# Optimization experiments

Measured on AMD Instinct MI355X. Metric: run time of the kernel, lower is better.

The kernel has to match this reference:

```python
import jax, jax.numpy as jnp
import numpy as np

# Architecture constants (from init_kwargs)
A, L, NCF = 200, 10, 9            # num_agent, in_len, num_control_features
D_MODEL, N_HEADS = 1024, 4
HEAD_DIM = D_MODEL // N_HEADS      # 256 (the module's 'head_dim')
PER_HEAD = HEAD_DIM // N_HEADS     # 64 (effective per-head dim after rearrange)
SCALE = HEAD_DIM ** -0.5           # module scales by head_dim**-0.5
N = A * L + NCF                    # 2009 tokens


def _build_mask():
    # block-diagonal agent mask: eye(A) repeat_interleaved L on both axes,
    # then zero-padded by NCF rows/cols for control features
    m = np.kron(np.eye(A, dtype=np.float32), np.ones((L, L), dtype=np.float32))
    m = np.pad(m, ((0, NCF), (0, NCF)))
    return jnp.asarray(m)  # [N, N]

_MASK = _build_mask()


def setup_inputs() -> dict:
    key = jax.random.key(0)
    k0, k1, k2, k3 = jax.random.split(key, 4)
    x = jax.random.normal(k0, (4, N, D_MODEL), jnp.float32)
    W_qkv = jax.random.normal(k1, (D_MODEL, HEAD_DIM * 3), jnp.float32) * 0.02
    W_qk_self = jax.random.normal(k2, (D_MODEL, HEAD_DIM * 2), jnp.float32) * 0.02
    W_out = jax.random.normal(k3, (HEAD_DIM, D_MODEL), jnp.float32) * 0.02
    b_out = jnp.zeros((D_MODEL,), jnp.float32)
    return {"x": x, "W_qkv": W_qkv, "W_qk_self": W_qk_self,
            "W_out": W_out, "b_out": b_out}


def _heads(t, b, n):
    # 'b n (h d) -> b h n d' with h = N_HEADS
    return t.reshape(b, n, N_HEADS, PER_HEAD).transpose(0, 2, 1, 3)


def reference(x, W_qkv, W_qk_self, W_out, b_out):
    b, n, _ = x.shape
    q, k, v = jnp.split(x @ W_qkv, 3, axis=-1)          # each [b, n, HEAD_DIM]
    q, k, v = _heads(q, b, n), _heads(k, b, n), _heads(v, b, n)  # [b,h,n,d]
    q_self, k_self = jnp.split(x @ W_qk_self, 2, axis=-1)
    q_self, k_self = _heads(q_self, b, n), _heads(k_self, b, n)

    dots = jnp.einsum('bhnd,bhmd->bhnm', q, k) * SCALE
    dots_self = jnp.einsum('bhnd,bhmd->bhnm', q_self, k_self) * SCALE
    dots_all = _MASK * dots_self + (1.0 - _MASK) * dots  # blend via block mask
    attn = jax.nn.softmax(dots_all, axis=-1)             # [b,h,n,n]

    out = jnp.einsum('bhnm,bhmd->bhnd', attn, v)
    out = out.transpose(0, 2, 1, 3).reshape(b, n, HEAD_DIM)  # 'b h n d -> b n (h d)'
    out = out @ W_out + b_out                            # to_out (dropout=0)
    return out, attn
```

## Files before the change

kernel.cpp:

```cpp
#include <hip/hip_runtime.h>

typedef unsigned short u16;
typedef unsigned int u32;
typedef short short8 __attribute__((ext_vector_type(8)));
typedef float f32x4 __attribute__((ext_vector_type(4)));
typedef float f32x16 __attribute__((ext_vector_type(16)));
typedef float float4a __attribute__((ext_vector_type(4), aligned(4)));

#define NTOK 2009
#define M8   8036
#define DMOD 1024
#define PKBH 129024

static __device__ __forceinline__ u16 f2bf(float f) {
  unsigned int x = __float_as_uint(f);
  x += 0x7fffu + ((x >> 16) & 1u);
  return (u16)(x >> 16);
}
static __device__ __forceinline__ float bf2f(u16 u) {
  return __uint_as_float((unsigned int)u << 16);
}
static __device__ __forceinline__ u32 pk2(float a, float b) {
  return (u32)f2bf(a) | ((u32)f2bf(b) << 16);
}
static __device__ __forceinline__ u32 cvtpk(float a, float b) {
  u32 d;
  asm("v_cvt_pk_bf16_f32 %0, %1, %2" : "=v"(d) : "v"(a), "v"(b));
  return d;
}

__global__ void k_conv_x(const float* __restrict__ x, u16* __restrict__ xb) {
  int i = blockIdx.x * 256 + threadIdx.x;
  float4 v = ((const float4*)x)[i];
  unsigned int a = (unsigned int)f2bf(v.x) | ((unsigned int)f2bf(v.y) << 16);
  unsigned int b = (unsigned int)f2bf(v.z) | ((unsigned int)f2bf(v.w) << 16);
  ((uint2*)xb)[i] = make_uint2(a, b);
}

__global__ void k_conv_wcat(const float* __restrict__ Wqkv, const float* __restrict__ Wqs,
                            u16* __restrict__ WtCat) {
  int i = blockIdx.x * 256 + threadIdx.x;
  int n = i >> 10, k = i & 1023;
  float v = (n < 768) ? Wqkv[k * 768 + n] : Wqs[k * 512 + (n - 768)];
  WtCat[i] = f2bf(v);
}

__global__ void k_conv_wout(const float* __restrict__ Wout, u16* __restrict__ WtOut) {
  int i = blockIdx.x * 256 + threadIdx.x;
  int n = i >> 8, k = i & 255;
  WtOut[i] = f2bf(Wout[k * 1024 + n]);
}

__global__ __launch_bounds__(256) void k_gemm_proj(
    const u16* __restrict__ A, const u16* __restrict__ Bt,
    u16* __restrict__ Qp, u16* __restrict__ Kp, u16* __restrict__ Vp,
    u16* __restrict__ Qsb, u16* __restrict__ Ksb)
{
  const int K = 1024;
  __shared__ u16 Al[64][72];
  __shared__ u16 Bl[64][72];
  int mt = blockIdx.x * 64, nt = blockIdx.y * 64;
  int tid = threadIdx.x; int lane = tid & 63, wave = tid >> 6;
  int fr = lane & 15, fk = (lane >> 4) * 8;
  f32x4 acc[4];
#pragma unroll
  for (int i = 0; i < 4; ++i) acc[i] = (f32x4){0.f, 0.f, 0.f, 0.f};
  for (int kt = 0; kt < K; kt += 64) {
#pragma unroll
    for (int r = 0; r < 2; ++r) {
      int c = tid + r * 256;
      int row = c >> 3, ch = (c & 7) * 8;
      int am = mt + row; if (am >= M8) am = 0;
      *(short8*)&Al[row][ch] = *(const short8*)&A[(size_t)am * K + kt + ch];
      *(short8*)&Bl[row][ch] = *(const short8*)&Bt[(size_t)(nt + row) * K + kt + ch];
    }
    __syncthreads();
#pragma unroll
    for (int cs = 0; cs < 2; ++cs) {
      short8 bfr = *(const short8*)&Bl[wave * 16 + fr][cs * 32 + fk];
#pragma unroll
      for (int mi = 0; mi < 4; ++mi) {
        short8 afr = *(const short8*)&Al[mi * 16 + fr][cs * 32 + fk];
        acc[mi] = __builtin_amdgcn_mfma_f32_16x16x32_bf16(afr, bfr, acc[mi], 0, 0, 0);
      }
    }
    __syncthreads();
  }
  int n = nt + wave * 16 + fr;
  int g = n >> 6, d = n & 63;
  int h = g & 3, sel = g >> 2;
  float scl = (sel == 0 || sel == 3) ? 0.0625f : 1.0f;
#pragma unroll
  for (int mi = 0; mi < 4; ++mi) {
#pragma unroll
    for (int i = 0; i < 4; ++i) {
      int m = mt + mi * 16 + (lane >> 4) * 4 + i;
      if (m >= M8) continue;
      int b_ = m / NTOK, tok = m - b_ * NTOK;
      int bh = b_ * 4 + h;
      u16 val = f2bf(acc[mi][i] * scl);
      if (sel <= 1) {
        u16* dst = sel == 0 ? Qp : Kp;
        size_t idx = ((((size_t)bh * 63 + (tok >> 5)) * 4 + (d >> 4)) * 2 + ((d >> 3) & 1)) * 256
                     + (tok & 31) * 8 + (d & 7);
        dst[idx] = val;
      } else if (sel == 2) {
        size_t idx = (((((size_t)bh * 63 + (tok >> 5)) * 2 + (d >> 5)) * 2 + ((tok >> 4) & 1)) * 2
                      + ((tok >> 3) & 1)) * 256 + (d & 31) * 8 + (tok & 7);
        Vp[idx] = val;
      } else {
        u16* p = (sel == 3) ? Qsb : Ksb;
        p[((size_t)bh * NTOK + tok) * 64 + d] = val;
      }
    }
  }
}

__global__ void k_self(const u16* __restrict__ Qs, const u16* __restrict__ Ks,
                       float* __restrict__ selfS) {
  int blk = blockIdx.x;
  int bh = blk / 200, a = blk % 200;
  int t = threadIdx.x;
  if (t >= 100) return;
  int ri = t / 10, rj = t % 10;
  const u16* qp = &Qs[((size_t)bh * NTOK + a * 10 + ri) * 64];
  const u16* kp = &Ks[((size_t)bh * NTOK + a * 10 + rj) * 64];
  float s = 0.f;
#pragma unroll 8
  for (int k = 0; k < 64; ++k) s += bf2f(qp[k]) * bf2f(kp[k]);
  selfS[(size_t)blk * 100 + t] = s;
}

__global__ __launch_bounds__(256, 2) void k_attn5(
    const u16* __restrict__ Qp, const u16* __restrict__ Kp,
    const u16* __restrict__ Vp, const float* __restrict__ selfS,
    float* __restrict__ attn, u16* __restrict__ Ob)
{
  __shared__ float s_sum[4][32];
  __shared__ float s_o[4][64][32];
  __shared__ float s_p[4][1024];
  int bh = blockIdx.x;
  int qt = blockIdx.y;
  int q0 = qt * 32;
  int tid = threadIdx.x;
  int lane = tid & 63, w = tid >> 6;
  int ql = lane & 31, h = lane >> 5;
  int qg = q0 + ql;
  int lo8 = ql * 8;

  const u16* qbase = Qp + (size_t)bh * PKBH + (size_t)qt * 2048;
  const u16* kbase = Kp + (size_t)bh * PKBH;
  const u16* vbase = Vp + (size_t)bh * PKBH;

  short8 qf[4];
#pragma unroll
  for (int c = 0; c < 4; ++c)
    qf[c] = *(const short8*)&qbase[(c * 2 + h) * 256 + lo8];

  int qa = (qg < 2000) ? (qg / 10) : -1;
  int band_lo = 1 << 30, band_hi = -(1 << 30);
  if (q0 < 2000) {
    int hi_row = (q0 + 31 < 1999) ? q0 + 31 : 1999;
    band_lo = (q0 / 10) * 10;
    band_hi = (hi_row / 10) * 10 + 10;
  }
  const float* sfb = &selfS[(size_t)bh * 20000];

  int t0 = w * 16;
  int t1 = t0 + 16; if (t1 > 63) t1 = 63;

  u32 pb[16][8];
  short8 kf[4], kfn[4];

#pragma unroll
  for (int c = 0; c < 4; ++c)
    kf[c] = *(const short8*)&kbase[(size_t)t0 * 2048 + (c * 2 + h) * 256 + lo8];
  float ssum = 0.f;
#pragma unroll
  for (int i = 0; i < 16; ++i) {
    int t = t0 + i;
    if (t < t1) {
      int tn = (t + 1 < t1) ? t + 1 : t0;
#pragma unroll
      for (int c = 0; c < 4; ++c)
        kfn[c] = *(const short8*)&kbase[(size_t)tn * 2048 + (c * 2 + h) * 256 + lo8];
      f32x16 acc = {};
#pragma unroll
      for (int c = 0; c < 4; ++c)
        acc = __builtin_amdgcn_mfma_f32_32x32x16_bf16(kf[c], qf[c], acc, 0, 0, 0);
      int kt = t * 32;
      float e[16];
      if ((kt < band_hi) && (kt + 32 > band_lo)) {
#pragma unroll
        for (int r = 0; r < 16; ++r) {
          int kc = kt + (r & 3) + 8 * (r >> 2) + 4 * h;
          float sc = acc[r];
          if (qa >= 0 && kc < 2000 && (kc / 10) == qa)
            sc = sfb[qa * 100 + (qg - qa * 10) * 10 + (kc - qa * 10)];
          e[r] = __expf(sc);
        }
      } else {
#pragma unroll
        for (int r = 0; r < 16; ++r) e[r] = __expf(acc[r]);
      }
      if (t == 62) {
#pragma unroll
        for (int r = 0; r < 16; ++r) {
          int kc = kt + (r & 3) + 8 * (r >> 2) + 4 * h;
          if (kc >= NTOK) e[r] = 0.f;
        }
      }
#pragma unroll
      for (int r2 = 0; r2 < 8; ++r2) {
        pb[i][r2] = cvtpk(e[2 * r2], e[2 * r2 + 1]);
        ssum += e[2 * r2] + e[2 * r2 + 1];
      }
#pragma unroll
      for (int c = 0; c < 4; ++c) kf[c] = kfn[c];
    }
  }
  ssum += __shfl_xor(ssum, 32);
  if (lane < 32) s_sum[w][ql] = ssum;
  __syncthreads();
  float inv = 1.0f / (s_sum[0][ql] + s_sum[1][ql] + s_sum[2][ql] + s_sum[3][ql]);

  f32x16 oacc0 = {}, oacc1 = {};
  short8 vf[4], vfn[4];
#pragma unroll
  for (int idx = 0; idx < 4; ++idx)
    vf[idx] = *(const short8*)&vbase[(size_t)t0 * 2048 + (idx * 2 + h) * 256 + lo8];

  char* pl = (char*)&s_p[w][0];

#pragma unroll
  for (int i = 0; i < 16; ++i) {
    int t = t0 + i;
    if (t < t1) {
      int tn = (t + 1 < t1) ? t + 1 : t0;
#pragma unroll
      for (int idx = 0; idx < 4; ++idx)
        vfn[idx] = *(const short8*)&vbase[(size_t)tn * 2048 + (idx * 2 + h) * 256 + lo8];
      int kt = t * 32;

#pragma unroll
      for (int rq = 0; rq < 4; ++rq) {
        u32 ua = pb[i][2 * rq], ub = pb[i][2 * rq + 1];
        f32x4 v = {__uint_as_float(ua << 16) * inv,
                   __uint_as_float(ua & 0xffff0000u) * inv,
                   __uint_as_float(ub << 16) * inv,
                   __uint_as_float(ub & 0xffff0000u) * inv};
        *(f32x4*)(pl + ql * 128 + ((rq * 32 + h * 16) ^ ((ql & 7) << 4))) = v;
      }
#pragma unroll
      for (int i2 = 0; i2 < 4; ++i2) {
        int r = i2 * 8 + (lane >> 3), ch = lane & 7;
        f32x4 v = *(f32x4*)(pl + r * 128 + ((ch * 16) ^ ((r & 7) << 4)));
        int grow = q0 + r;
        int col0 = kt + ch * 4;
        if (grow < NTOK) {
          float* arow = &attn[((size_t)bh * NTOK + grow) * NTOK];
          if (col0 + 3 < NTOK) {
            *(float4a*)&arow[col0] = (float4a){v[0], v[1], v[2], v[3]};
          } else {
#pragma unroll
            for (int j = 0; j < 4; ++j)
              if (col0 + j < NTOK) arow[col0 + j] = v[j];
          }
        }
      }

      u32 p00 = __shfl_xor(pb[i][0], 32), p01 = __shfl_xor(pb[i][1], 32);
      u32 p10 = __shfl_xor(pb[i][2], 32), p11 = __shfl_xor(pb[i][3], 32);
      u32 p20 = __shfl_xor(pb[i][4], 32), p21 = __shfl_xor(pb[i][5], 32);
      u32 p30 = __shfl_xor(pb[i][6], 32), p31 = __shfl_xor(pb[i][7], 32);
      u32 b0[4], b1[4];
      b0[0] = h ? p10 : pb[i][0];  b0[1] = h ? p11 : pb[i][1];
      b0[2] = h ? pb[i][2] : p00;  b0[3] = h ? pb[i][3] : p01;
      b1[0] = h ? p30 : pb[i][4];  b1[1] = h ? p31 : pb[i][5];
      b1[2] = h ? pb[i][6] : p20;  b1[3] = h ? pb[i][7] : p21;
      short8 B0, B1;
      __builtin_memcpy(&B0, b0, 16);
      __builtin_memcpy(&B1, b1, 16);
      oacc0 = __builtin_amdgcn_mfma_f32_32x32x16_bf16(vf[0], B0, oacc0, 0, 0, 0);
      oacc1 = __builtin_amdgcn_mfma_f32_32x32x16_bf16(vf[2], B0, oacc1, 0, 0, 0);
      oacc0 = __builtin_amdgcn_mfma_f32_32x32x16_bf16(vf[1], B1, oacc0, 0, 0, 0);
      oacc1 = __builtin_amdgcn_mfma_f32_32x32x16_bf16(vf[3], B1, oacc1, 0, 0, 0);
#pragma unroll
      for (int c = 0; c < 4; ++c) vf[c] = vfn[c];
    }
  }

#pragma unroll
  for (int r = 0; r < 16; ++r) {
    int d = (r & 3) + 8 * (r >> 2) + 4 * h;
    s_o[w][d][ql] = oacc0[r];
    s_o[w][d + 32][ql] = oacc1[r];
  }
  __syncthreads();
  {
    int q = tid & 31, dg = tid >> 5;
    int qg2 = q0 + q;
    if (qg2 < NTOK) {
      float invq = 1.0f / (s_sum[0][q] + s_sum[1][q] + s_sum[2][q] + s_sum[3][q]);
      int b_ = bh >> 2, hd = bh & 3;
      u16* orow = &Ob[((size_t)(b_ * NTOK + qg2)) * 256 + hd * 64 + dg * 8];
      u32 wpk[4];
#pragma unroll
      for (int j = 0; j < 4; ++j) {
        int d = dg * 8 + 2 * j;
        float a = (s_o[0][d][q] + s_o[1][d][q] + s_o[2][d][q] + s_o[3][d][q]) * invq;
        float b = (s_o[0][d + 1][q] + s_o[1][d + 1][q] + s_o[2][d + 1][q] + s_o[3][d + 1][q]) * invq;
        wpk[j] = pk2(a, b);
      }
      *(uint4*)orow = make_uint4(wpk[0], wpk[1], wpk[2], wpk[3]);
    }
  }
}

__global__ __launch_bounds__(256) void k_gemm_out(
    const u16* __restrict__ A, const u16* __restrict__ Bt,
    const float* __restrict__ bias, float* __restrict__ C)
{
  const int K = 256;
  __shared__ u16 Al[64][72];
  __shared__ u16 Bl[64][72];
  int mt = blockIdx.x * 64, nt = blockIdx.y * 64;
  int tid = threadIdx.x; int lane = tid & 63, wave = tid >> 6;
  int fr = lane & 15, fk = (lane >> 4) * 8;
  f32x4 acc[4];
#pragma unroll
  for (int i = 0; i < 4; ++i) acc[i] = (f32x4){0.f, 0.f, 0.f, 0.f};
  for (int kt = 0; kt < K; kt += 64) {
#pragma unroll
    for (int r = 0; r < 2; ++r) {
      int c = tid + r * 256;
      int row = c >> 3, ch = (c & 7) * 8;
      int am = mt + row; if (am >= M8) am = 0;
      *(short8*)&Al[row][ch] = *(const short8*)&A[(size_t)am * K + kt + ch];
      *(short8*)&Bl[row][ch] = *(const short8*)&Bt[(size_t)(nt + row) * K + kt + ch];
    }
    __syncthreads();
#pragma unroll
    for (int cs = 0; cs < 2; ++cs) {
      short8 bfr = *(const short8*)&Bl[wave * 16 + fr][cs * 32 + fk];
#pragma unroll
      for (int mi = 0; mi < 4; ++mi) {
        short8 afr = *(const short8*)&Al[mi * 16 + fr][cs * 32 + fk];
        acc[mi] = __builtin_amdgcn_mfma_f32_16x16x32_bf16(afr, bfr, acc[mi], 0, 0, 0);
      }
    }
    __syncthreads();
  }
  int n = nt + wave * 16 + fr;
  float bn = bias[n];
#pragma unroll
  for (int mi = 0; mi < 4; ++mi) {
#pragma unroll
    for (int i = 0; i < 4; ++i) {
      int m = mt + mi * 16 + (lane >> 4) * 4 + i;
      if (m < M8) C[(size_t)m * DMOD + n] = acc[mi][i] + bn;
    }
  }
}

extern "C" void kernel_launch(void* const* d_in, const int* in_sizes, int n_in,
                              void* d_out, int out_size, void* d_ws, size_t ws_size,
                              hipStream_t stream) {
  (void)in_sizes; (void)n_in; (void)out_size; (void)ws_size;
  const float* x    = (const float*)d_in[0];
  const float* Wqkv = (const float*)d_in[1];
  const float* Wqs  = (const float*)d_in[2];
  const float* Wout = (const float*)d_in[3];
  const float* bout = (const float*)d_in[4];
  float* out  = (float*)d_out;
  float* attn = out + (size_t)M8 * DMOD;

  char* ws = (char*)d_ws;
  u16*   xb    = (u16*)(ws);
  u16*   WtCat = (u16*)(ws + 16457728);
  u16*   WtOut = (u16*)(ws + 19079168);
  u16*   Qp    = (u16*)(ws + 19603456);
  u16*   Kp    = (u16*)(ws + 23732224);
  u16*   Vp    = (u16*)(ws + 27860992);
  u16*   Qsb   = (u16*)(ws + 31989760);
  u16*   Ksb   = (u16*)(ws + 36104192);
  u16*   Ob    = (u16*)(ws + 40218624);
  float* selfS = (float*)(ws + 44333056);

  k_conv_x<<<dim3(8036), dim3(256), 0, stream>>>(x, xb);
  k_conv_wcat<<<dim3(5120), dim3(256), 0, stream>>>(Wqkv, Wqs, WtCat);
  k_conv_wout<<<dim3(1024), dim3(256), 0, stream>>>(Wout, WtOut);
  k_gemm_proj<<<dim3(126, 20), dim3(256), 0, stream>>>(xb, WtCat, Qp, Kp, Vp, Qsb, Ksb);
  k_self<<<dim3(3200), dim3(128), 0, stream>>>(Qsb, Ksb, selfS);
  k_attn5<<<dim3(16, 63), dim3(256), 0, stream>>>(Qp, Kp, Vp, selfS, attn, Ob);
  k_gemm_out<<<dim3(126, 16), dim3(256), 0, stream>>>(Ob, WtOut, bout, out);
}
```

Baseline: 218.9 us.

## Split softmax row sums into separate pass and enlarge GEMM tiles

Both projection GEMMs move to 128x128 tiles with a 2x2 wave grid and load operands straight into LDS with global_load_lds. This raises data reuse per tile and removes the register round trip on the way to shared memory. The attention kernel no longer holds a 16x8 register buffer of probabilities across two passes. A new k_sums kernel computes the softmax denominators first, so k_attn6 can write normalized attention and accumulate PV in one pass. The cost is recomputing QK^T and exp twice, plus one extra launch that reuses the start of the xb workspace.

```diff
diff --git a/kernel.cpp b/kernel.cpp
--- a/kernel.cpp
+++ b/kernel.cpp
@@ -28,6 +28,11 @@
   asm("v_cvt_pk_bf16_f32 %0, %1, %2" : "=v"(d) : "v"(a), "v"(b));
   return d;
 }
+static __device__ __forceinline__ void gload_lds16(const void* g, void* l) {
+  __builtin_amdgcn_global_load_lds(
+      (const __attribute__((address_space(1))) void*)g,
+      (__attribute__((address_space(3))) void*)l, 16, 0, 0);
+}
 
 __global__ void k_conv_x(const float* __restrict__ x, u16* __restrict__ xb) {
   int i = blockIdx.x * 256 + threadIdx.x;
@@ -56,61 +61,74 @@
     u16* __restrict__ Qp, u16* __restrict__ Kp, u16* __restrict__ Vp,
     u16* __restrict__ Qsb, u16* __restrict__ Ksb)
 {
-  const int K = 1024;
-  __shared__ u16 Al[64][72];
-  __shared__ u16 Bl[64][72];
-  int mt = blockIdx.x * 64, nt = blockIdx.y * 64;
-  int tid = threadIdx.x; int lane = tid & 63, wave = tid >> 6;
-  int fr = lane & 15, fk = (lane >> 4) * 8;
-  f32x4 acc[4];
-#pragma unroll
-  for (int i = 0; i < 4; ++i) acc[i] = (f32x4){0.f, 0.f, 0.f, 0.f};
-  for (int kt = 0; kt < K; kt += 64) {
-#pragma unroll
-    for (int r = 0; r < 2; ++r) {
-      int c = tid + r * 256;
-      int row = c >> 3, ch = (c & 7) * 8;
-      int am = mt + row; if (am >= M8) am = 0;
-      *(short8*)&Al[row][ch] = *(const short8*)&A[(size_t)am * K + kt + ch];
-      *(short8*)&Bl[row][ch] = *(const short8*)&Bt[(size_t)(nt + row) * K + kt + ch];
+  __shared__ u16 Asm[128 * 64];
+  __shared__ u16 Bsm[128 * 64];
+  int mt = blockIdx.x * 128, nt = blockIdx.y * 128;
+  int tid = threadIdx.x, lane = tid & 63, w = tid >> 6;
+  int wm = w >> 1, wn = w & 1;
+  int fr = lane & 15, fq = lane >> 4;
+  int srow = w * 32 + (lane >> 3);
+  int scol = (lane & 7) * 8;
+  f32x4 acc[4][4];
+#pragma unroll
+  for (int a = 0; a < 4; ++a)
+#pragma unroll
+    for (int b = 0; b < 4; ++b) acc[a][b] = (f32x4){0.f, 0.f, 0.f, 0.f};
+
+  for (int kt = 0; kt < 1024; kt += 64) {
+#pragma unroll
+    for (int j = 0; j < 4; ++j) {
+      int r = srow + j * 8;
+      int am = mt + r; if (am >= M8) am = 0;
+      gload_lds16(A + (size_t)am * 1024 + kt + scol, Asm + (size_t)(w * 32 + j * 8) * 64);
+      gload_lds16(Bt + (size_t)(nt + r) * 1024 + kt + scol, Bsm + (size_t)(w * 32 + j * 8) * 64);
     }
     __syncthreads();
 #pragma unroll
     for (int cs = 0; cs < 2; ++cs) {
-      short8 bfr = *(const short8*)&Bl[wave * 16 + fr][cs * 32 + fk];
-#pragma unroll
-      for (int mi = 0; mi < 4; ++mi) {
-        short8 afr = *(const short8*)&Al[mi * 16 + fr][cs * 32 + fk];
-        acc[mi] = __builtin_amdgcn_mfma_f32_16x16x32_bf16(afr, bfr, acc[mi], 0, 0, 0);
-      }
+      short8 af[4], bf[4];
+#pragma unroll
+      for (int i = 0; i < 4; ++i) {
+        af[i] = *(const short8*)&Asm[(size_t)(wm * 64 + i * 16 + fr) * 64 + cs * 32 + fq * 8];
+        bf[i] = *(const short8*)&Bsm[(size_t)(wn * 64 + i * 16 + fr) * 64 + cs * 32 + fq * 8];
+      }
+#pragma unroll
+      for (int mi = 0; mi < 4; ++mi)
+#pragma unroll
+        for (int ni = 0; ni < 4; ++ni)
+          acc[mi][ni] = __builtin_amdgcn_mfma_f32_16x16x32_bf16(af[mi], bf[ni], acc[mi][ni], 0, 0, 0);
     }
     __syncthreads();
   }
-  int n = nt + wave * 16 + fr;
-  int g = n >> 6, d = n & 63;
-  int h = g & 3, sel = g >> 2;
-  float scl = (sel == 0 || sel == 3) ? 0.0625f : 1.0f;
-#pragma unroll
-  for (int mi = 0; mi < 4; ++mi) {
-#pragma unroll
-    for (int i = 0; i < 4; ++i) {
-      int m = mt + mi * 16 + (lane >> 4) * 4 + i;
-      if (m >= M8) continue;
-      int b_ = m / NTOK, tok = m - b_ * NTOK;
-      int bh = b_ * 4 + h;
-      u16 val = f2bf(acc[mi][i] * scl);
-      if (sel <= 1) {
-        u16* dst = sel == 0 ? Qp : Kp;
-        size_t idx = ((((size_t)bh * 63 + (tok >> 5)) * 4 + (d >> 4)) * 2 + ((d >> 3) & 1)) * 256
-                     + (tok & 31) * 8 + (d & 7);
-        dst[idx] = val;
-      } else if (sel == 2) {
-        size_t idx = (((((size_t)bh * 63 + (tok >> 5)) * 2 + (d >> 5)) * 2 + ((tok >> 4) & 1)) * 2
-                      + ((tok >> 3) & 1)) * 256 + (d & 31) * 8 + (tok & 7);
-        Vp[idx] = val;
-      } else {
-        u16* p = (sel == 3) ? Qsb : Ksb;
-        p[((size_t)bh * NTOK + tok) * 64 + d] = val;
+
+#pragma unroll
+  for (int ni = 0; ni < 4; ++ni) {
+    int n = nt + wn * 64 + ni * 16 + fr;
+    int g = n >> 6, d = n & 63;
+    int h = g & 3, sel = g >> 2;
+    float scl = (sel == 0 || sel == 3) ? 0.0625f : 1.0f;
+#pragma unroll
+    for (int mi = 0; mi < 4; ++mi) {
+#pragma unroll
+      for (int i = 0; i < 4; ++i) {
+        int m = mt + wm * 64 + mi * 16 + fq * 4 + i;
+        if (m >= M8) continue;
+        int b_ = m / NTOK, tok = m - b_ * NTOK;
+        int bh = b_ * 4 + h;
+        u16 val = f2bf(acc[mi][ni][i] * scl);
+        if (sel <= 1) {
+          u16* dst = sel == 0 ? Qp : Kp;
+          size_t idx = ((((size_t)bh * 63 + (tok >> 5)) * 4 + (d >> 4)) * 2 + ((d >> 3) & 1)) * 256
+                       + (tok & 31) * 8 + (d & 7);
+          dst[idx] = val;
+        } else if (sel == 2) {
+          size_t idx = (((((size_t)bh * 63 + (tok >> 5)) * 2 + (d >> 5)) * 2 + ((tok >> 4) & 1)) * 2
+                        + ((tok >> 3) & 1)) * 256 + (d & 31) * 8 + (tok & 7);
+          Vp[idx] = val;
+        } else {
+          u16* p = (sel == 3) ? Qsb : Ksb;
+          p[((size_t)bh * NTOK + tok) * 64 + d] = val;
+        }
       }
     }
   }
@@ -131,12 +149,88 @@
   selfS[(size_t)blk * 100 + t] = s;
 }
 
-__global__ __launch_bounds__(256, 2) void k_attn5(
+__global__ __launch_bounds__(256) void k_sums(
+    const u16* __restrict__ Qp, const u16* __restrict__ Kp,
+    const float* __restrict__ selfS, float* __restrict__ sums)
+{
+  int bh = blockIdx.x, qt = blockIdx.y;
+  int tid = threadIdx.x, lane = tid & 63, w = tid >> 6;
+  int ks = blockIdx.z * 4 + w;
+  int ql = lane & 31, h = lane >> 5;
+  int q0 = qt * 32, qg = q0 + ql;
+  int lo8 = ql * 8;
+
+  const u16* qbase = Qp + (size_t)bh * PKBH + (size_t)qt * 2048;
+  const u16* kbase = Kp + (size_t)bh * PKBH;
+
+  short8 qf[4];
+#pragma unroll
+  for (int c = 0; c < 4; ++c)
+    qf[c] = *(const short8*)&qbase[(c * 2 + h) * 256 + lo8];
+
+  int qa = (qg < 2000) ? (qg / 10) : -1;
+  int band_lo = 1 << 30, band_hi = -(1 << 30);
+  if (q0 < 2000) {
+    int hi_row = (q0 + 31 < 1999) ? q0 + 31 : 1999;
+    band_lo = (q0 / 10) * 10;
+    band_hi = (hi_row / 10) * 10 + 10;
+  }
+  const float* sfb = &selfS[(size_t)bh * 20000];
+
+  int t0 = ks * 8;
+  int t1 = t0 + 8; if (t1 > 63) t1 = 63;
+
+  short8 kf[4], kfn[4];
+#pragma unroll
+  for (int c = 0; c < 4; ++c)
+    kf[c] = *(const short8*)&kbase[(size_t)t0 * 2048 + (c * 2 + h) * 256 + lo8];
+  float ssum = 0.f;
+  for (int t = t0; t < t1; ++t) {
+    int tn = (t + 1 < t1) ? t + 1 : t0;
+#pragma unroll
+    for (int c = 0; c < 4; ++c)
+      kfn[c] = *(const short8*)&kbase[(size_t)tn * 2048 + (c * 2 + h) * 256 + lo8];
+    f32x16 acc = {};
+#pragma unroll
+    for (int c = 0; c < 4; ++c)
+      acc = __builtin_amdgcn_mfma_f32_32x32x16_bf16(kf[c], qf[c], acc, 0, 0, 0);
+    int kt = t * 32;
+    float e[16];
+    if ((kt < band_hi) && (kt + 32 > band_lo)) {
+#pragma unroll
+      for (int r = 0; r < 16; ++r) {
+        int kc = kt + (r & 3) + 8 * (r >> 2) + 4 * h;
+        float sc = acc[r];
+        if (qa >= 0 && kc < 2000 && (kc / 10) == qa)
+          sc = sfb[qa * 100 + (qg - qa * 10) * 10 + (kc - qa * 10)];
+        e[r] = __expf(sc);
+      }
+    } else {
+#pragma unroll
+      for (int r = 0; r < 16; ++r) e[r] = __expf(acc[r]);
+    }
+    if (t == 62) {
+#pragma unroll
+      for (int r = 0; r < 16; ++r) {
+        int kc = kt + (r & 3) + 8 * (r >> 2) + 4 * h;
+        if (kc >= NTOK) e[r] = 0.f;
+      }
+    }
+#pragma unroll
+    for (int r = 0; r < 16; ++r) ssum += e[r];
+#pragma unroll
+    for (int c = 0; c < 4; ++c) kf[c] = kfn[c];
+  }
+  ssum += __shfl_xor(ssum, 32);
+  if (lane < 32) sums[((size_t)(bh * 63 + qt) * 8 + ks) * 32 + ql] = ssum;
+}
+
+__global__ __launch_bounds__(256, 2) void k_attn6(
     const u16* __restrict__ Qp, const u16* __restrict__ Kp,
     const u16* __restrict__ Vp, const float* __restrict__ selfS,
+    const float* __restrict__ sums,
     float* __restrict__ attn, u16* __restrict__ Ob)
 {
-  __shared__ float s_sum[4][32];
   __shared__ float s_o[4][64][32];
   __shared__ float s_p[4][1024];
   int bh = blockIdx.x;
@@ -148,6 +242,12 @@
   int qg = q0 + ql;
   int lo8 = ql * 8;
 
+  const float* sp = &sums[(size_t)(bh * 63 + qt) * 256 + ql];
+  float tot = 0.f;
+#pragma unroll
+  for (int ks = 0; ks < 8; ++ks) tot += sp[ks * 32];
+  float inv = 1.0f / tot;
+
   const u16* qbase = Qp + (size_t)bh * PKBH + (size_t)qt * 2048;
   const u16* kbase = Kp + (size_t)bh * PKBH;
   const u16* vbase = Vp + (size_t)bh * PKBH;
@@ -169,125 +269,95 @@
   int t0 = w * 16;
   int t1 = t0 + 16; if (t1 > 63) t1 = 63;
 
-  u32 pb[16][8];
-  short8 kf[4], kfn[4];
-
-#pragma unroll
-  for (int c = 0; c < 4; ++c)
+  f32x16 oacc0 = {}, oacc1 = {};
+  short8 kf[4], kfn[4], vf[4], vfn[4];
+#pragma unroll
+  for (int c = 0; c < 4; ++c) {
     kf[c] = *(const short8*)&kbase[(size_t)t0 * 2048 + (c * 2 + h) * 256 + lo8];
-  float ssum = 0.f;
-#pragma unroll
-  for (int i = 0; i < 16; ++i) {
-    int t = t0 + i;
-    if (t < t1) {
-      int tn = (t + 1 < t1) ? t + 1 : t0;
-#pragma unroll
-      for (int c = 0; c < 4; ++c)
-        kfn[c] = *(const short8*)&kbase[(size_t)tn * 2048 + (c * 2 + h) * 256 + lo8];
-      f32x16 acc = {};
-#pragma unroll
-      for (int c = 0; c < 4; ++c)
-        acc = __builtin_amdgcn_mfma_f32_32x32x16_bf16(kf[c], qf[c], acc, 0, 0, 0);
-      int kt = t * 32;
-      float e[16];
-      if ((kt < band_hi) && (kt + 32 > band_lo)) {
-#pragma unroll
-        for (int r = 0; r < 16; ++r) {
-          int kc = kt + (r & 3) + 8 * (r >> 2) + 4 * h;
-          float sc = acc[r];
-          if (qa >= 0 && kc < 2000 && (kc / 10) == qa)
-            sc = sfb[qa * 100 + (qg - qa * 10) * 10 + (kc - qa * 10)];
-          e[r] = __expf(sc);
+    vf[c] = *(const short8*)&vbase[(size_t)t0 * 2048 + (c * 2 + h) * 256 + lo8];
+  }
+  char* pl = (char*)&s_p[w][0];
+
+  for (int t = t0; t < t1; ++t) {
+    int tn = (t + 1 < t1) ? t + 1 : t0;
+#pragma unroll
+    for (int c = 0; c < 4; ++c) {
+      kfn[c] = *(const short8*)&kbase[(size_t)tn * 2048 + (c * 2 + h) * 256 + lo8];
+      vfn[c] = *(const short8*)&vbase[(size_t)tn * 2048 + (c * 2 + h) * 256 + lo8];
+    }
+    f32x16 acc = {};
+#pragma unroll
+    for (int c = 0; c < 4; ++c)
+      acc = __builtin_amdgcn_mfma_f32_32x32x16_bf16(kf[c], qf[c], acc, 0, 0, 0);
+    int kt = t * 32;
+    float p[16];
+    if ((kt < band_hi) && (kt + 32 > band_lo)) {
+#pragma unroll
+      for (int r = 0; r < 16; ++r) {
+        int kc = kt + (r & 3) + 8 * (r >> 2) + 4 * h;
+        float sc = acc[r];
+        if (qa >= 0 && kc < 2000 && (kc / 10) == qa)
+          sc = sfb[qa * 100 + (qg - qa * 10) * 10 + (kc - qa * 10)];
+        p[r] = __expf(sc);
+      }
+    } else {
+#pragma unroll
+      for (int r = 0; r < 16; ++r) p[r] = __expf(acc[r]);
+    }
+    if (t == 62) {
+#pragma unroll
+      for (int r = 0; r < 16; ++r) {
+        int kc = kt + (r & 3) + 8 * (r >> 2) + 4 * h;
+        if (kc >= NTOK) p[r] = 0.f;
+      }
+    }
+#pragma unroll
+    for (int r = 0; r < 16; ++r) p[r] *= inv;
+
+#pragma unroll
+    for (int rq = 0; rq < 4; ++rq) {
+      f32x4 v = {p[4 * rq], p[4 * rq + 1], p[4 * rq + 2], p[4 * rq + 3]};
+      *(f32x4*)(pl + ql * 128 + ((rq * 32 + h * 16) ^ ((ql & 7) << 4))) = v;
+    }
+#pragma unroll
+    for (int i2 = 0; i2 < 4; ++i2) {
+      int r = i2 * 8 + (lane >> 3), ch = lane & 7;
+      f32x4 v = *(f32x4*)(pl + r * 128 + ((ch * 16) ^ ((r & 7) << 4)));
+      int grow = q0 + r;
+      int col0 = kt + ch * 4;
+      if (grow < NTOK) {
+        float* arow = &attn[((size_t)bh * NTOK + grow) * NTOK];
+        if (col0 + 3 < NTOK) {
+          *(float4a*)&arow[col0] = (float4a){v[0], v[1], v[2], v[3]};
+        } else {
+#pragma unroll
+          for (int j = 0; j < 4; ++j)
+            if (col0 + j < NTOK) arow[col0 + j] = v[j];
         }
-      } else {
-#pragma unroll
-        for (int r = 0; r < 16; ++r) e[r] = __expf(acc[r]);
-      }
-      if (t == 62) {
-#pragma unroll
-        for (int r = 0; r < 16; ++r) {
-          int kc = kt + (r & 3) + 8 * (r >> 2) + 4 * h;
-          if (kc >= NTOK) e[r] = 0.f;
-        }
-      }
-#pragma unroll
-      for (int r2 = 0; r2 < 8; ++r2) {
-        pb[i][r2] = cvtpk(e[2 * r2], e[2 * r2 + 1]);
-        ssum += e[2 * r2] + e[2 * r2 + 1];
-      }
-#pragma unroll
-      for (int c = 0; c < 4; ++c) kf[c] = kfn[c];
-    }
-  }
-  ssum += __shfl_xor(ssum, 32);
-  if (lane < 32) s_sum[w][ql] = ssum;
-  __syncthreads();
-  float inv = 1.0f / (s_sum[0][ql] + s_sum[1][ql] + s_sum[2][ql] + s_sum[3][ql]);
-
-  f32x16 oacc0 = {}, oacc1 = {};
-  short8 vf[4], vfn[4];
-#pragma unroll
-  for (int idx = 0; idx < 4; ++idx)
-    vf[idx] = *(const short8*)&vbase[(size_t)t0 * 2048 + (idx * 2 + h) * 256 + lo8];
-
-  char* pl = (char*)&s_p[w][0];
-
-#pragma unroll
-  for (int i = 0; i < 16; ++i) {
-    int t = t0 + i;
-    if (t < t1) {
-      int tn = (t + 1 < t1) ? t + 1 : t0;
-#pragma unroll
-      for (int idx = 0; idx < 4; ++idx)
-        vfn[idx] = *(const short8*)&vbase[(size_t)tn * 2048 + (idx * 2 + h) * 256 + lo8];
-      int kt = t * 32;
-
-#pragma unroll
-      for (int rq = 0; rq < 4; ++rq) {
-        u32 ua = pb[i][2 * rq], ub = pb[i][2 * rq + 1];
-        f32x4 v = {__uint_as_float(ua << 16) * inv,
-                   __uint_as_float(ua & 0xffff0000u) * inv,
-                   __uint_as_float(ub << 16) * inv,
-                   __uint_as_float(ub & 0xffff0000u) * inv};
-        *(f32x4*)(pl + ql * 128 + ((rq * 32 + h * 16) ^ ((ql & 7) << 4))) = v;
-      }
-#pragma unroll
-      for (int i2 = 0; i2 < 4; ++i2) {
-        int r = i2 * 8 + (lane >> 3), ch = lane & 7;
-        f32x4 v = *(f32x4*)(pl + r * 128 + ((ch * 16) ^ ((r & 7) << 4)));
-        int grow = q0 + r;
-        int col0 = kt + ch * 4;
-        if (grow < NTOK) {
-          float* arow = &attn[((size_t)bh * NTOK + grow) * NTOK];
-          if (col0 + 3 < NTOK) {
-            *(float4a*)&arow[col0] = (float4a){v[0], v[1], v[2], v[3]};
-          } else {
-#pragma unroll
-            for (int j = 0; j < 4; ++j)
-              if (col0 + j < NTOK) arow[col0 + j] = v[j];
-          }
-        }
-      }
-
-      u32 p00 = __shfl_xor(pb[i][0], 32), p01 = __shfl_xor(pb[i][1], 32);
-      u32 p10 = __shfl_xor(pb[i][2], 32), p11 = __shfl_xor(pb[i][3], 32);
-      u32 p20 = __shfl_xor(pb[i][4], 32), p21 = __shfl_xor(pb[i][5], 32);
-      u32 p30 = __shfl_xor(pb[i][6], 32), p31 = __shfl_xor(pb[i][7], 32);
-      u32 b0[4], b1[4];
-      b0[0] = h ? p10 : pb[i][0];  b0[1] = h ? p11 : pb[i][1];
-      b0[2] = h ? pb[i][2] : p00;  b0[3] = h ? pb[i][3] : p01;
-      b1[0] = h ? p30 : pb[i][4];  b1[1] = h ? p31 : pb[i][5];
-      b1[2] = h ? pb[i][6] : p20;  b1[3] = h ? pb[i][7] : p21;
-      short8 B0, B1;
-      __builtin_memcpy(&B0, b0, 16);
-      __builtin_memcpy(&B1, b1, 16);
-      oacc0 = __builtin_amdgcn_mfma_f32_32x32x16_bf16(vf[0], B0, oacc0, 0, 0, 0);
-      oacc1 = __builtin_amdgcn_mfma_f32_32x32x16_bf16(vf[2], B0, oacc1, 0, 0, 0);
-      oacc0 = __builtin_amdgcn_mfma_f32_32x32x16_bf16(vf[1], B1, oacc0, 0, 0, 0);
-      oacc1 = __builtin_amdgcn_mfma_f32_32x32x16_bf16(vf[3], B1, oacc1, 0, 0, 0);
-#pragma unroll
-      for (int c = 0; c < 4; ++c) vf[c] = vfn[c];
-    }
+      }
+    }
+
+    u32 pk[8];
+#pragma unroll
+    for (int r2 = 0; r2 < 8; ++r2) pk[r2] = cvtpk(p[2 * r2], p[2 * r2 + 1]);
+    u32 p00 = __shfl_xor(pk[0], 32), p01 = __shfl_xor(pk[1], 32);
+    u32 p10 = __shfl_xor(pk[2], 32), p11 = __shfl_xor(pk[3], 32);
+    u32 p20 = __shfl_xor(pk[4], 32), p21 = __shfl_xor(pk[5], 32);
+    u32 p30 = __shfl_xor(pk[6], 32), p31 = __shfl_xor(pk[7], 32);
+    u32 b0[4], b1[4];
+    b0[0] = h ? p10 : pk[0];  b0[1] = h ? p11 : pk[1];
+    b0[2] = h ? pk[2] : p00;  b0[3] = h ? pk[3] : p01;
+    b1[0] = h ? p30 : pk[4];  b1[1] = h ? p31 : pk[5];
+    b1[2] = h ? pk[6] : p20;  b1[3] = h ? pk[7] : p21;
+    short8 B0, B1;
+    __builtin_memcpy(&B0, b0, 16);
+    __builtin_memcpy(&B1, b1, 16);
+    oacc0 = __builtin_amdgcn_mfma_f32_32x32x16_bf16(vf[0], B0, oacc0, 0, 0, 0);
+    oacc1 = __builtin_amdgcn_mfma_f32_32x32x16_bf16(vf[2], B0, oacc1, 0, 0, 0);
+    oacc0 = __builtin_amdgcn_mfma_f32_32x32x16_bf16(vf[1], B1, oacc0, 0, 0, 0);
+    oacc1 = __builtin_amdgcn_mfma_f32_32x32x16_bf16(vf[3], B1, oacc1, 0, 0, 0);
+#pragma unroll
+    for (int c = 0; c < 4; ++c) { kf[c] = kfn[c]; vf[c] = vfn[c]; }
   }
 
 #pragma unroll
@@ -301,15 +371,14 @@
     int q = tid & 31, dg = tid >> 5;
     int qg2 = q0 + q;
     if (qg2 < NTOK) {
-      float invq = 1.0f / (s_sum[0][q] + s_sum[1][q] + s_sum[2][q] + s_sum[3][q]);
       int b_ = bh >> 2, hd = bh & 3;
       u16* orow = &Ob[((size_t)(b_ * NTOK + qg2)) * 256 + hd * 64 + dg * 8];
       u32 wpk[4];
 #pragma unroll
       for (int j = 0; j < 4; ++j) {
         int d = dg * 8 + 2 * j;
-        float a = (s_o[0][d][q] + s_o[1][d][q] + s_o[2][d][q] + s_o[3][d][q]) * invq;
-        float b = (s_o[0][d + 1][q] + s_o[1][d + 1][q] + s_o[2][d + 1][q] + s_o[3][d + 1][q]) * invq;
+        float a = s_o[0][d][q] + s_o[1][d][q] + s_o[2][d][q] + s_o[3][d][q];
+        float b = s_o[0][d + 1][q] + s_o[1][d + 1][q] + s_o[2][d + 1][q] + s_o[3][d + 1][q];
         wpk[j] = pk2(a, b);
       }
       *(uint4*)orow = make_uint4(wpk[0], wpk[1], wpk[2], wpk[3]);
@@ -321,45 +390,57 @@
     const u16* __restrict__ A, const u16* __restrict__ Bt,
     const float* __restrict__ bias, float* __restrict__ C)
 {
-  const int K = 256;
-  __shared__ u16 Al[64][72];
-  __shared__ u16 Bl[64][72];
-  int mt = blockIdx.x * 64, nt = blockIdx.y * 64;
-  int tid = threadIdx.x; int lane = tid & 63, wave = tid >> 6;
-  int fr = lane & 15, fk = (lane >> 4) * 8;
-  f32x4 acc[4];
-#pragma unroll
-  for (int i = 0; i < 4; ++i) acc[i] = (f32x4){0.f, 0.f, 0.f, 0.f};
-  for (int kt = 0; kt < K; kt += 64) {
-#pragma unroll
-    for (int r = 0; r < 2; ++r) {
-      int c = tid + r * 256;
-      int row = c >> 3, ch = (c & 7) * 8;
-      int am = mt + row; if (am >= M8) am = 0;
-      *(short8*)&Al[row][ch] = *(const short8*)&A[(size_t)am * K + kt + ch];
-      *(short8*)&Bl[row][ch] = *(const short8*)&Bt[(size_t)(nt + row) * K + kt + ch];
+  __shared__ u16 Asm[128 * 64];
+  __shared__ u16 Bsm[128 * 64];
+  int mt = blockIdx.x * 128, nt = blockIdx.y * 128;
+  int tid = threadIdx.x, lane = tid & 63, w = tid >> 6;
+  int wm = w >> 1, wn = w & 1;
+  int fr = lane & 15, fq = lane >> 4;
+  int srow = w * 32 + (lane >> 3);
+  int scol = (lane & 7) * 8;
+  f32x4 acc[4][4];
+#pragma unroll
+  for (int a = 0; a < 4; ++a)
+#pragma unroll
+    for (int b = 0; b < 4; ++b) acc[a][b] = (f32x4){0.f, 0.f, 0.f, 0.f};
+
+  for (int kt = 0; kt < 256; kt += 64) {
+#pragma unroll
+    for (int j = 0; j < 4; ++j) {
+      int r = srow + j * 8;
+      int am = mt + r; if (am >= M8) am = 0;
+      gload_lds16(A + (size_t)am * 256 + kt + scol, Asm + (size_t)(w * 32 + j * 8) * 64);
+      gload_lds16(Bt + (size_t)(nt + r) * 256 + kt + scol, Bsm + (size_t)(w * 32 + j * 8) * 64);
     }
     __syncthreads();
 #pragma unroll
     for (int cs = 0; cs < 2; ++cs) {
-      short8 bfr = *(const short8*)&Bl[wave * 16 + fr][cs * 32 + fk];
-#pragma unroll
-      for (int mi = 0; mi < 4; ++mi) {
-        short8 afr = *(const short8*)&Al[mi * 16 + fr][cs * 32 + fk];
-        acc[mi] = __builtin_amdgcn_mfma_f32_16x16x32_bf16(afr, bfr, acc[mi], 0, 0, 0);
-      }
+      short8 af[4], bf[4];
+#pragma unroll
+      for (int i = 0; i < 4; ++i) {
+        af[i] = *(const short8*)&Asm[(size_t)(wm * 64 + i * 16 + fr) * 64 + cs * 32 + fq * 8];
+        bf[i] = *(const short8*)&Bsm[(size_t)(wn * 64 + i * 16 + fr) * 64 + cs * 32 + fq * 8];
+      }
+#pragma unroll
+      for (int mi = 0; mi < 4; ++mi)
+#pragma unroll
+        for (int ni = 0; ni < 4; ++ni)
+          acc[mi][ni] = __builtin_amdgcn_mfma_f32_16x16x32_bf16(af[mi], bf[ni], acc[mi][ni], 0, 0, 0);
     }
     __syncthreads();
   }
-  int n = nt + wave * 16 + fr;
-  float bn = bias[n];
-#pragma unroll
-  for (int mi = 0; mi < 4; ++mi) {
-#pragma unroll
-    for (int i = 0; i < 4; ++i) {
-      int m = mt + mi * 16 + (lane >> 4) * 4 + i;
-      if (m < M8) C[(size_t)m * DMOD + n] = acc[mi][i] + bn;
-    }
+
+#pragma unroll
+  for (int ni = 0; ni < 4; ++ni) {
+    int n = nt + wn * 64 + ni * 16 + fr;
+    float bn = bias[n];
+#pragma unroll
+    for (int mi = 0; mi < 4; ++mi)
+#pragma unroll
+      for (int i = 0; i < 4; ++i) {
+        int m = mt + wm * 64 + mi * 16 + fq * 4 + i;
+        if (m < M8) C[(size_t)m * DMOD + n] = acc[mi][ni][i] + bn;
+      }
   }
 }
 
@@ -386,12 +467,14 @@
   u16*   Ksb   = (u16*)(ws + 36104192);
   u16*   Ob    = (u16*)(ws + 40218624);
   float* selfS = (float*)(ws + 44333056);
+  float* sums  = (float*)(ws);
 
   k_conv_x<<<dim3(8036), dim3(256), 0, stream>>>(x, xb);
   k_conv_wcat<<<dim3(5120), dim3(256), 0, stream>>>(Wqkv, Wqs, WtCat);
   k_conv_wout<<<dim3(1024), dim3(256), 0, stream>>>(Wout, WtOut);
-  k_gemm_proj<<<dim3(126, 20), dim3(256), 0, stream>>>(xb, WtCat, Qp, Kp, Vp, Qsb, Ksb);
+  k_gemm_proj<<<dim3(63, 10), dim3(256), 0, stream>>>(xb, WtCat, Qp, Kp, Vp, Qsb, Ksb);
   k_self<<<dim3(3200), dim3(128), 0, stream>>>(Qsb, Ksb, selfS);
-  k_attn5<<<dim3(16, 63), dim3(256), 0, stream>>>(Qp, Kp, Vp, selfS, attn, Ob);
-  k_gemm_out<<<dim3(126, 16), dim3(256), 0, stream>>>(Ob, WtOut, bout, out);
-}
+  k_sums<<<dim3(16, 63, 2), dim3(256), 0, stream>>>(Qp, Kp, selfS, sums);
+  k_attn6<<<dim3(16, 63), dim3(256), 0, stream>>>(Qp, Kp, Vp, selfS, sums, attn, Ob);
+  k_gemm_out<<<dim3(63, 8), dim3(256), 0, stream>>>(Ob, WtOut, bout, out);
+}
```

Measured after the change: 239.9 us. +9.6%, slower.

## Enlarge GEMM tiles to 128x128 with direct global-to-LDS loads, nontemporal stores

Applied to the files above, without the earlier changes.

Both projection and output GEMMs move from 64x64 to 128x128 block tiles, with each wave computing a 64x64 sub-tile. Tiles are staged through global_load_lds (direct global-to-LDS) instead of register round-trips. The large attn matrix and the output use nontemporal stores to reduce cache pollution. The larger tiles raise data reuse but increase register pressure, cut the grid size (fewer blocks for occupancy), and drop the LDS row padding, which may cause bank conflicts.

```diff
diff --git a/kernel.cpp b/kernel.cpp
--- a/kernel.cpp
+++ b/kernel.cpp
@@ -28,6 +28,11 @@
   asm("v_cvt_pk_bf16_f32 %0, %1, %2" : "=v"(d) : "v"(a), "v"(b));
   return d;
 }
+static __device__ __forceinline__ void gload_lds16(const void* g, void* l) {
+  __builtin_amdgcn_global_load_lds(
+      (const __attribute__((address_space(1))) void*)g,
+      (__attribute__((address_space(3))) void*)l, 16, 0, 0);
+}
 
 __global__ void k_conv_x(const float* __restrict__ x, u16* __restrict__ xb) {
   int i = blockIdx.x * 256 + threadIdx.x;
@@ -56,61 +61,74 @@
     u16* __restrict__ Qp, u16* __restrict__ Kp, u16* __restrict__ Vp,
     u16* __restrict__ Qsb, u16* __restrict__ Ksb)
 {
-  const int K = 1024;
-  __shared__ u16 Al[64][72];
-  __shared__ u16 Bl[64][72];
-  int mt = blockIdx.x * 64, nt = blockIdx.y * 64;
-  int tid = threadIdx.x; int lane = tid & 63, wave = tid >> 6;
-  int fr = lane & 15, fk = (lane >> 4) * 8;
-  f32x4 acc[4];
-#pragma unroll
-  for (int i = 0; i < 4; ++i) acc[i] = (f32x4){0.f, 0.f, 0.f, 0.f};
-  for (int kt = 0; kt < K; kt += 64) {
-#pragma unroll
-    for (int r = 0; r < 2; ++r) {
-      int c = tid + r * 256;
-      int row = c >> 3, ch = (c & 7) * 8;
-      int am = mt + row; if (am >= M8) am = 0;
-      *(short8*)&Al[row][ch] = *(const short8*)&A[(size_t)am * K + kt + ch];
-      *(short8*)&Bl[row][ch] = *(const short8*)&Bt[(size_t)(nt + row) * K + kt + ch];
+  __shared__ u16 Asm[128 * 64];
+  __shared__ u16 Bsm[128 * 64];
+  int mt = blockIdx.x * 128, nt = blockIdx.y * 128;
+  int tid = threadIdx.x, lane = tid & 63, w = tid >> 6;
+  int wm = w >> 1, wn = w & 1;
+  int fr = lane & 15, fq = lane >> 4;
+  int srow = w * 32 + (lane >> 3);
+  int scol = (lane & 7) * 8;
+  f32x4 acc[4][4];
+#pragma unroll
+  for (int a = 0; a < 4; ++a)
+#pragma unroll
+    for (int b = 0; b < 4; ++b) acc[a][b] = (f32x4){0.f, 0.f, 0.f, 0.f};
+
+  for (int kt = 0; kt < 1024; kt += 64) {
+#pragma unroll
+    for (int j = 0; j < 4; ++j) {
+      int r = srow + j * 8;
+      int am = mt + r; if (am >= M8) am = 0;
+      gload_lds16(A + (size_t)am * 1024 + kt + scol, Asm + (size_t)(w * 32 + j * 8) * 64);
+      gload_lds16(Bt + (size_t)(nt + r) * 1024 + kt + scol, Bsm + (size_t)(w * 32 + j * 8) * 64);
     }
     __syncthreads();
 #pragma unroll
     for (int cs = 0; cs < 2; ++cs) {
-      short8 bfr = *(const short8*)&Bl[wave * 16 + fr][cs * 32 + fk];
-#pragma unroll
-      for (int mi = 0; mi < 4; ++mi) {
-        short8 afr = *(const short8*)&Al[mi * 16 + fr][cs * 32 + fk];
-        acc[mi] = __builtin_amdgcn_mfma_f32_16x16x32_bf16(afr, bfr, acc[mi], 0, 0, 0);
-      }
+      short8 af[4], bf[4];
+#pragma unroll
+      for (int i = 0; i < 4; ++i) {
+        af[i] = *(const short8*)&Asm[(size_t)(wm * 64 + i * 16 + fr) * 64 + cs * 32 + fq * 8];
+        bf[i] = *(const short8*)&Bsm[(size_t)(wn * 64 + i * 16 + fr) * 64 + cs * 32 + fq * 8];
+      }
+#pragma unroll
+      for (int mi = 0; mi < 4; ++mi)
+#pragma unroll
+        for (int ni = 0; ni < 4; ++ni)
+          acc[mi][ni] = __builtin_amdgcn_mfma_f32_16x16x32_bf16(af[mi], bf[ni], acc[mi][ni], 0, 0, 0);
     }
     __syncthreads();
   }
-  int n = nt + wave * 16 + fr;
-  int g = n >> 6, d = n & 63;
-  int h = g & 3, sel = g >> 2;
-  float scl = (sel == 0 || sel == 3) ? 0.0625f : 1.0f;
-#pragma unroll
-  for (int mi = 0; mi < 4; ++mi) {
-#pragma unroll
-    for (int i = 0; i < 4; ++i) {
-      int m = mt + mi * 16 + (lane >> 4) * 4 + i;
-      if (m >= M8) continue;
-      int b_ = m / NTOK, tok = m - b_ * NTOK;
-      int bh = b_ * 4 + h;
-      u16 val = f2bf(acc[mi][i] * scl);
-      if (sel <= 1) {
-        u16* dst = sel == 0 ? Qp : Kp;
-        size_t idx = ((((size_t)bh * 63 + (tok >> 5)) * 4 + (d >> 4)) * 2 + ((d >> 3) & 1)) * 256
-                     + (tok & 31) * 8 + (d & 7);
-        dst[idx] = val;
-      } else if (sel == 2) {
-        size_t idx = (((((size_t)bh * 63 + (tok >> 5)) * 2 + (d >> 5)) * 2 + ((tok >> 4) & 1)) * 2
-                      + ((tok >> 3) & 1)) * 256 + (d & 31) * 8 + (tok & 7);
-        Vp[idx] = val;
-      } else {
-        u16* p = (sel == 3) ? Qsb : Ksb;
-        p[((size_t)bh * NTOK + tok) * 64 + d] = val;
+
+#pragma unroll
+  for (int ni = 0; ni < 4; ++ni) {
+    int n = nt + wn * 64 + ni * 16 + fr;
+    int g = n >> 6, d = n & 63;
+    int h = g & 3, sel = g >> 2;
+    float scl = (sel == 0 || sel == 3) ? 0.0625f : 1.0f;
+#pragma unroll
+    for (int mi = 0; mi < 4; ++mi) {
+#pragma unroll
+      for (int i = 0; i < 4; ++i) {
+        int m = mt + wm * 64 + mi * 16 + fq * 4 + i;
+        if (m >= M8) continue;
+        int b_ = m / NTOK, tok = m - b_ * NTOK;
+        int bh = b_ * 4 + h;
+        u16 val = f2bf(acc[mi][ni][i] * scl);
+        if (sel <= 1) {
+          u16* dst = sel == 0 ? Qp : Kp;
+          size_t idx = ((((size_t)bh * 63 + (tok >> 5)) * 4 + (d >> 4)) * 2 + ((d >> 3) & 1)) * 256
+                       + (tok & 31) * 8 + (d & 7);
+          dst[idx] = val;
+        } else if (sel == 2) {
+          size_t idx = (((((size_t)bh * 63 + (tok >> 5)) * 2 + (d >> 5)) * 2 + ((tok >> 4) & 1)) * 2
+                        + ((tok >> 3) & 1)) * 256 + (d & 31) * 8 + (tok & 7);
+          Vp[idx] = val;
+        } else {
+          u16* p = (sel == 3) ? Qsb : Ksb;
+          p[((size_t)bh * NTOK + tok) * 64 + d] = val;
+        }
       }
     }
   }
@@ -131,7 +149,7 @@
   selfS[(size_t)blk * 100 + t] = s;
 }
 
-__global__ __launch_bounds__(256, 2) void k_attn5(
+__global__ __launch_bounds__(256, 2) void k_attn7(
     const u16* __restrict__ Qp, const u16* __restrict__ Kp,
     const u16* __restrict__ Vp, const float* __restrict__ selfS,
     float* __restrict__ attn, u16* __restrict__ Ob)
@@ -260,11 +278,13 @@
         if (grow < NTOK) {
           float* arow = &attn[((size_t)bh * NTOK + grow) * NTOK];
           if (col0 + 3 < NTOK) {
-            *(float4a*)&arow[col0] = (float4a){v[0], v[1], v[2], v[3]};
+            __builtin_nontemporal_store((float4a){v[0], v[1], v[2], v[3]},
+                                        (float4a*)&arow[col0]);
           } else {
 #pragma unroll
             for (int j = 0; j < 4; ++j)
-              if (col0 + j < NTOK) arow[col0 + j] = v[j];
+              if (col0 + j < NTOK)
+                __builtin_nontemporal_store(v[j], &arow[col0 + j]);
           }
         }
       }
@@ -321,45 +341,58 @@
     const u16* __restrict__ A, const u16* __restrict__ Bt,
     const float* __restrict__ bias, float* __restrict__ C)
 {
-  const int K = 256;
-  __shared__ u16 Al[64][72];
-  __shared__ u16 Bl[64][72];
-  int mt = blockIdx.x * 64, nt = blockIdx.y * 64;
-  int tid = threadIdx.x; int lane = tid & 63, wave = tid >> 6;
-  int fr = lane & 15, fk = (lane >> 4) * 8;
-  f32x4 acc[4];
-#pragma unroll
-  for (int i = 0; i < 4; ++i) acc[i] = (f32x4){0.f, 0.f, 0.f, 0.f};
-  for (int kt = 0; kt < K; kt += 64) {
-#pragma unroll
-    for (int r = 0; r < 2; ++r) {
-      int c = tid + r * 256;
-      int row = c >> 3, ch = (c & 7) * 8;
-      int am = mt + row; if (am >= M8) am = 0;
-      *(short8*)&Al[row][ch] = *(const short8*)&A[(size_t)am * K + kt + ch];
-      *(short8*)&Bl[row][ch] = *(const short8*)&Bt[(size_t)(nt + row) * K + kt + ch];
+  __shared__ u16 Asm[128 * 64];
+  __shared__ u16 Bsm[128 * 64];
+  int mt = blockIdx.x * 128, nt = blockIdx.y * 128;
+  int tid = threadIdx.x, lane = tid & 63, w = tid >> 6;
+  int wm = w >> 1, wn = w & 1;
+  int fr = lane & 15, fq = lane >> 4;
+  int srow = w * 32 + (lane >> 3);
+  int scol = (lane & 7) * 8;
+  f32x4 acc[4][4];
+#pragma unroll
+  for (int a = 0; a < 4; ++a)
+#pragma unroll
+    for (int b = 0; b < 4; ++b) acc[a][b] = (f32x4){0.f, 0.f, 0.f, 0.f};
+
+  for (int kt = 0; kt < 256; kt += 64) {
+#pragma unroll
+    for (int j = 0; j < 4; ++j) {
+      int r = srow + j * 8;
+      int am = mt + r; if (am >= M8) am = 0;
+      gload_lds16(A + (size_t)am * 256 + kt + scol, Asm + (size_t)(w * 32 + j * 8) * 64);
+      gload_lds16(Bt + (size_t)(nt + r) * 256 + kt + scol, Bsm + (size_t)(w * 32 + j * 8) * 64);
     }
     __syncthreads();
 #pragma unroll
     for (int cs = 0; cs < 2; ++cs) {
-      short8 bfr = *(const short8*)&Bl[wave * 16 + fr][cs * 32 + fk];
-#pragma unroll
-      for (int mi = 0; mi < 4; ++mi) {
-        short8 afr = *(const short8*)&Al[mi * 16 + fr][cs * 32 + fk];
-        acc[mi] = __builtin_amdgcn_mfma_f32_16x16x32_bf16(afr, bfr, acc[mi], 0, 0, 0);
-      }
+      short8 af[4], bf[4];
+#pragma unroll
+      for (int i = 0; i < 4; ++i) {
+        af[i] = *(const short8*)&Asm[(size_t)(wm * 64 + i * 16 + fr) * 64 + cs * 32 + fq * 8];
+        bf[i] = *(const short8*)&Bsm[(size_t)(wn * 64 + i * 16 + fr) * 64 + cs * 32 + fq * 8];
+      }
+#pragma unroll
+      for (int mi = 0; mi < 4; ++mi)
+#pragma unroll
+        for (int ni = 0; ni < 4; ++ni)
+          acc[mi][ni] = __builtin_amdgcn_mfma_f32_16x16x32_bf16(af[mi], bf[ni], acc[mi][ni], 0, 0, 0);
     }
     __syncthreads();
   }
-  int n = nt + wave * 16 + fr;
-  float bn = bias[n];
-#pragma unroll
-  for (int mi = 0; mi < 4; ++mi) {
-#pragma unroll
-    for (int i = 0; i < 4; ++i) {
-      int m = mt + mi * 16 + (lane >> 4) * 4 + i;
-      if (m < M8) C[(size_t)m * DMOD + n] = acc[mi][i] + bn;
-    }
+
+#pragma unroll
+  for (int ni = 0; ni < 4; ++ni) {
+    int n = nt + wn * 64 + ni * 16 + fr;
+    float bn = bias[n];
+#pragma unroll
+    for (int mi = 0; mi < 4; ++mi)
+#pragma unroll
+      for (int i = 0; i < 4; ++i) {
+        int m = mt + wm * 64 + mi * 16 + fq * 4 + i;
+        if (m < M8)
+          __builtin_nontemporal_store(acc[mi][ni][i] + bn, &C[(size_t)m * DMOD + n]);
+      }
   }
 }
 
@@ -390,8 +423,8 @@
   k_conv_x<<<dim3(8036), dim3(256), 0, stream>>>(x, xb);
   k_conv_wcat<<<dim3(5120), dim3(256), 0, stream>>>(Wqkv, Wqs, WtCat);
   k_conv_wout<<<dim3(1024), dim3(256), 0, stream>>>(Wout, WtOut);
-  k_gemm_proj<<<dim3(126, 20), dim3(256), 0, stream>>>(xb, WtCat, Qp, Kp, Vp, Qsb, Ksb);
+  k_gemm_proj<<<dim3(63, 10), dim3(256), 0, stream>>>(xb, WtCat, Qp, Kp, Vp, Qsb, Ksb);
   k_self<<<dim3(3200), dim3(128), 0, stream>>>(Qsb, Ksb, selfS);
-  k_attn5<<<dim3(16, 63), dim3(256), 0, stream>>>(Qp, Kp, Vp, selfS, attn, Ob);
-  k_gemm_out<<<dim3(126, 16), dim3(256), 0, stream>>>(Ob, WtOut, bout, out);
-}
+  k_attn7<<<dim3(16, 63), dim3(256), 0, stream>>>(Qp, Kp, Vp, selfS, attn, Ob);
+  k_gemm_out<<<dim3(63, 8), dim3(256), 0, stream>>>(Ob, WtOut, bout, out);
+}
```

Measured after the change: 327.0 us. 1.49x slower.
